# Kernel tuning notes

Measured on AMD Instinct MI355X. Metric: run time of the kernel, lower is better.

## Reference

```python
import jax, jax.numpy as jnp
import numpy as np

D = 1024

def setup_inputs() -> dict:
    key = jax.random.key(0)
    kx, kw = jax.random.split(key)
    x = jax.random.normal(kx, (4, 2048, D), dtype=jnp.float32)
    # nn.Linear(d, 3d, bias=False): weight [3d, d]; y = x @ W.T
    W = jax.random.normal(kw, (3 * D, D), dtype=jnp.float32) * (1.0 / np.sqrt(D))
    return {"x": x, "W": W}

def reference(x, W):
    d = x.shape[-1]
    qkv = jnp.einsum('bsd,ed->bse', x, W)  # [B,S,3d]
    q, k, v = jnp.split(qkv, 3, axis=2)
    att = jnp.einsum('bqd,bkd->bqk', q, k) * (1.0 / jnp.sqrt(jnp.asarray(d, x.dtype)))
    att = jax.nn.softmax(att, axis=-1)
    y = jnp.einsum('bqk,bkd->bqd', att, v)
    return y
```

## Files before the change

kernel.cpp:

```cpp
#include <hip/hip_runtime.h>
#include <hip/hip_bf16.h>

typedef __attribute__((ext_vector_type(8))) short short8;
typedef __attribute__((ext_vector_type(4))) float f32x4;

typedef unsigned short u16;

__device__ __forceinline__ u16 f32_to_bf16(float f) {
    unsigned int u = __float_as_uint(f);
    u += 0x7fffu + ((u >> 16) & 1u);
    return (u16)(u >> 16);
}

__device__ __forceinline__ void gload16(const u16* g, u16* lds_base) {
    __builtin_amdgcn_global_load_lds(
        (const __attribute__((address_space(1))) void*)g,
        (__attribute__((address_space(3))) void*)lds_base, 16, 0, 0);
}

__device__ __forceinline__ void phase_bar() {
    __builtin_amdgcn_s_barrier();
    __builtin_amdgcn_sched_barrier(0);
}
__device__ __forceinline__ void wait_vm8() {
    asm volatile("s_waitcnt vmcnt(8)" ::: "memory");
    __builtin_amdgcn_sched_barrier(0);
}
__device__ __forceinline__ void wait_vm7() {
    asm volatile("s_waitcnt vmcnt(7)" ::: "memory");
    __builtin_amdgcn_sched_barrier(0);
}
__device__ __forceinline__ void wait_vm0() {
    asm volatile("s_waitcnt vmcnt(0)" ::: "memory");
    __builtin_amdgcn_sched_barrier(0);
}

__global__ void cast_inputs(const float* __restrict__ x, u16* __restrict__ Xb,
                            const float* __restrict__ W, u16* __restrict__ Wb,
                            float* __restrict__ l,
                            int nx4, int nw4, int nl) {
    int i = blockIdx.x * blockDim.x + threadIdx.x;
    if (i >= nx4 + nw4) {
        int idx = i - (nx4 + nw4);
        if (idx < nl) l[idx] = 0.f;
        return;
    }
    const float* in; u16* out; int idx;
    if (i < nx4) { in = x; out = Xb; idx = i; }
    else { idx = i - nx4; in = W; out = Wb; }
    float4 v = ((const float4*)in)[idx];
    ushort4 o;
    o.x = f32_to_bf16(v.x); o.y = f32_to_bf16(v.y);
    o.z = f32_to_bf16(v.z); o.w = f32_to_bf16(v.w);
    ((ushort4*)out)[idx] = o;
}


struct Acc256 { f32x4 acc[8][4]; };
struct Acc192 { f32x4 acc[8][3]; };

template<int MH>
__device__ __forceinline__ void rd_a(const u16* __restrict__ sA, int wr, int lane,
                                     int lr, short8 (&af)[4][2]) {
#pragma unroll
    for (int a2 = 0; a2 < 4; ++a2) {
        const int row = wr * 128 + MH * 64 + a2 * 16 + lr;
#pragma unroll
        for (int k2 = 0; k2 < 2; ++k2) {
            const int cb = (lane >> 4) + k2 * 4;
            af[a2][k2] = *(const short8*)(sA + row * 64 + ((cb ^ (lr & 7)) * 8));
        }
    }
}

template<int NH>
__device__ __forceinline__ void rd_b(const u16* __restrict__ sB, int wc, int lane,
                                     int lr, short8 (&bf)[2][2]) {
#pragma unroll
    for (int b2 = 0; b2 < 2; ++b2) {
        const int row = wc * 64 + NH * 32 + b2 * 16 + lr;
#pragma unroll
        for (int k2 = 0; k2 < 2; ++k2) {
            const int cb = (lane >> 4) + k2 * 4;
            bf[b2][k2] = *(const short8*)(sB + row * 64 + ((cb ^ (lr & 7)) * 8));
        }
    }
}

template<int MH, int NH>
__device__ __forceinline__ void mm_q(Acc256& fr, const short8 (&af)[4][2],
                                     const short8 (&bf)[2][2]) {
    __builtin_amdgcn_s_setprio(1);
#pragma unroll
    for (int a2 = 0; a2 < 4; ++a2)
#pragma unroll
        for (int b2 = 0; b2 < 2; ++b2)
#pragma unroll
            for (int k2 = 0; k2 < 2; ++k2)
                fr.acc[MH * 4 + a2][NH * 2 + b2] =
                    __builtin_amdgcn_mfma_f32_16x16x32_bf16(
                        af[a2][k2], bf[b2][k2],
                        fr.acc[MH * 4 + a2][NH * 2 + b2], 0, 0, 0);
    __builtin_amdgcn_s_setprio(0);
}

__device__ __forceinline__ void rd_b01(const u16* __restrict__ sB, int wc, int lane,
                                       int lr, short8 (&bf)[2][2]) {
#pragma unroll
    for (int b2 = 0; b2 < 2; ++b2) {
        const int row = wc * 48 + b2 * 16 + lr;
#pragma unroll
        for (int k2 = 0; k2 < 2; ++k2) {
            const int cb = (lane >> 4) + k2 * 4;
            bf[b2][k2] = *(const short8*)(sB + row * 64 + ((cb ^ (lr & 7)) * 8));
        }
    }
}

__device__ __forceinline__ void rd_b2(const u16* __restrict__ sB, int wc, int lane,
                                      int lr, short8 (&bf)[2]) {
    const int row = wc * 48 + 32 + lr;
#pragma unroll
    for (int k2 = 0; k2 < 2; ++k2) {
        const int cb = (lane >> 4) + k2 * 4;
        bf[k2] = *(const short8*)(sB + row * 64 + ((cb ^ (lr & 7)) * 8));
    }
}

template<int MH>
__device__ __forceinline__ void mm_b01(Acc192& fr, const short8 (&af)[4][2],
                                       const short8 (&bf)[2][2]) {
    __builtin_amdgcn_s_setprio(1);
#pragma unroll
    for (int a2 = 0; a2 < 4; ++a2)
#pragma unroll
        for (int b2 = 0; b2 < 2; ++b2)
#pragma unroll
            for (int k2 = 0; k2 < 2; ++k2)
                fr.acc[MH * 4 + a2][b2] =
                    __builtin_amdgcn_mfma_f32_16x16x32_bf16(
                        af[a2][k2], bf[b2][k2],
                        fr.acc[MH * 4 + a2][b2], 0, 0, 0);
    __builtin_amdgcn_s_setprio(0);
}

template<int MH>
__device__ __forceinline__ void mm_b2(Acc192& fr, const short8 (&af)[4][2],
                                      const short8 (&bf)[2]) {
    __builtin_amdgcn_s_setprio(1);
#pragma unroll
    for (int a2 = 0; a2 < 4; ++a2)
#pragma unroll
        for (int k2 = 0; k2 < 2; ++k2)
            fr.acc[MH * 4 + a2][2] =
                __builtin_amdgcn_mfma_f32_16x16x32_bf16(
                    af[a2][k2], bf[k2], fr.acc[MH * 4 + a2][2], 0, 0, 0);
    __builtin_amdgcn_s_setprio(0);
}

__device__ __forceinline__ void gemm_core_256(
    const u16* __restrict__ A, const u16* __restrict__ Bt,
    int K, int lda, int ldb, int row0, int col0, u16* sm, Acc256& fr)
{
    const int t    = threadIdx.x;
    const int lane = t & 63;
    const int wave = t >> 6;
    const int wr   = wave >> 2;
    const int wc   = wave & 3;
    const int lr   = lane & 15;
    const int srow = lane >> 3;
    const int gc   = (lane & 7) ^ srow;

    const u16* const sA0 = sm;
    const u16* const sA1 = sm + 16384;
    const u16* const sB0 = sm + 32768;
    const u16* const sB1 = sm + 49152;

#pragma unroll
    for (int a = 0; a < 8; ++a)
#pragma unroll
        for (int b = 0; b < 4; ++b)
            fr.acc[a][b] = (f32x4){0.f, 0.f, 0.f, 0.f};

    const u16* aB = A  + (long long)(row0 + wave * 8 + srow) * lda + gc * 8;
    const u16* bB = Bt + (long long)(col0 + wave * 8 + srow) * ldb + gc * 8;
    u16* const sAw = sm + wave * 512;
    u16* const sBw = sm + 32768 + wave * 512;

    auto stageA = [&](int kt) {
        u16* d = sAw + (kt & 1) * 16384;
        const u16* g = aB + kt * 64;
#pragma unroll
        for (int r4 = 0; r4 < 4; ++r4)
            gload16(g + (long long)(r4 * 64) * lda, d + r4 * 4096);
    };
    auto stageB = [&](int kt) {
        u16* d = sBw + (kt & 1) * 16384;
        const u16* g = bB + kt * 64;
#pragma unroll
        for (int r4 = 0; r4 < 4; ++r4)
            gload16(g + (long long)(r4 * 64) * ldb, d + r4 * 4096);
    };

    stageA(0); stageB(0); stageA(1); stageB(1);
    wait_vm8();
    phase_bar();

    const int NI = K >> 7;
    short8 af[4][2], bfa[2][2], bfb[2][2];
#pragma unroll 1
    for (int i = 0; i < NI; ++i) {
        const bool more = (i + 1 < NI);
        const int t2 = 2 * i + 2;

        rd_a<0>(sA0, wr, lane, lr, af);
        rd_b<0>(sB0, wc, lane, lr, bfa);
        phase_bar();
        mm_q<0, 0>(fr, af, bfa);
        phase_bar();

        rd_b<1>(sB0, wc, lane, lr, bfb);
        phase_bar();
        mm_q<0, 1>(fr, af, bfb);
        phase_bar();

        rd_a<1>(sA0, wr, lane, lr, af);
        if (more) stageB(t2);
        phase_bar();
        mm_q<1, 1>(fr, af, bfb);
        phase_bar();

        if (more) stageA(t2);
        phase_bar();
        mm_q<1, 0>(fr, af, bfa);
        if (more) wait_vm8(); else wait_vm0();
        phase_bar();

        rd_a<0>(sA1, wr, lane, lr, af);
        rd_b<0>(sB1, wc, lane, lr, bfa);
        phase_bar();
        mm_q<0, 0>(fr, af, bfa);
        phase_bar();

        rd_b<1>(sB1, wc, lane, lr, bfb);
        phase_bar();
        mm_q<0, 1>(fr, af, bfb);
        phase_bar();

        rd_a<1>(sA1, wr, lane, lr, af);
        if (more) stageB(t2 + 1);
        phase_bar();
        mm_q<1, 1>(fr, af, bfb);
        phase_bar();

        if (more) stageA(t2 + 1);
        phase_bar();
        mm_q<1, 0>(fr, af, bfa);
        if (more) wait_vm8();
        phase_bar();
    }
}

__device__ __forceinline__ void gemm_core_192(
    const u16* __restrict__ A, const u16* __restrict__ Bt,
    int K, int lda, int ldb, int row0, int col0, u16* sm, Acc192& fr)
{
    const int t    = threadIdx.x;
    const int lane = t & 63;
    const int wave = t >> 6;
    const int wr   = wave >> 2;
    const int wc   = wave & 3;
    const int lr   = lane & 15;
    const int srow = lane >> 3;
    const int gc   = (lane & 7) ^ srow;

    const u16* const sA0 = sm;
    const u16* const sA1 = sm + 16384;
    const u16* const sB0 = sm + 32768;
    const u16* const sB1 = sm + 45056;

#pragma unroll
    for (int a = 0; a < 8; ++a)
#pragma unroll
        for (int b = 0; b < 3; ++b)
            fr.acc[a][b] = (f32x4){0.f, 0.f, 0.f, 0.f};

    const u16* aB = A  + (long long)(row0 + wave * 8 + srow) * lda + gc * 8;
    const u16* bB = Bt + (long long)(col0 + wave * 8 + srow) * ldb + gc * 8;
    u16* const sAw = sm + wave * 512;
    u16* const sBw = sm + 32768 + wave * 512;

    auto stageA = [&](int kt) {
        u16* d = sAw + (kt & 1) * 16384;
        const u16* g = aB + kt * 64;
#pragma unroll
        for (int r4 = 0; r4 < 4; ++r4)
            gload16(g + (long long)(r4 * 64) * lda, d + r4 * 4096);
    };
    auto stageB = [&](int kt) {
        u16* d = sBw + (kt & 1) * 12288;
        const u16* g = bB + kt * 64;
#pragma unroll
        for (int r4 = 0; r4 < 3; ++r4)
            gload16(g + (long long)(r4 * 64) * ldb, d + r4 * 4096);
    };

    stageA(0); stageB(0); stageA(1); stageB(1);
    wait_vm7();
    phase_bar();

    const int NI = K >> 7;
    short8 af[4][2], bfa[2][2], bfb[2];
#pragma unroll 1
    for (int i = 0; i < NI; ++i) {
        const bool more = (i + 1 < NI);
        const int t2 = 2 * i + 2;

        rd_a<0>(sA0, wr, lane, lr, af);
        rd_b01(sB0, wc, lane, lr, bfa);
        phase_bar();
        mm_b01<0>(fr, af, bfa);
        phase_bar();

        rd_b2(sB0, wc, lane, lr, bfb);
        phase_bar();
        mm_b2<0>(fr, af, bfb);
        phase_bar();

        rd_a<1>(sA0, wr, lane, lr, af);
        if (more) stageB(t2);
        phase_bar();
        mm_b2<1>(fr, af, bfb);
        phase_bar();

        if (more) stageA(t2);
        phase_bar();
        mm_b01<1>(fr, af, bfa);
        if (more) wait_vm7(); else wait_vm0();
        phase_bar();

        rd_a<0>(sA1, wr, lane, lr, af);
        rd_b01(sB1, wc, lane, lr, bfa);
        phase_bar();
        mm_b01<0>(fr, af, bfa);
        phase_bar();

        rd_b2(sB1, wc, lane, lr, bfb);
        phase_bar();
        mm_b2<0>(fr, af, bfb);
        phase_bar();

        rd_a<1>(sA1, wr, lane, lr, af);
        if (more) stageB(t2 + 1);
        phase_bar();
        mm_b2<1>(fr, af, bfb);
        phase_bar();

        if (more) stageA(t2 + 1);
        phase_bar();
        mm_b01<1>(fr, af, bfa);
        if (more) wait_vm7();
        phase_bar();
    }
}


__global__ __launch_bounds__(512, 1) void gemm_qkv(
    const u16* __restrict__ Xb, const u16* __restrict__ Wb,
    u16* __restrict__ QK, u16* __restrict__ VT)
{
    __shared__ u16 sm[57344];
    const int row0 = blockIdx.y * 256;
    const int col0 = blockIdx.x * 192;

    Acc192 fr;
    gemm_core_192(Xb, Wb, 1024, 1024, 1024, row0, col0, sm, fr);

    const int lane = threadIdx.x & 63;
    const int wave = threadIdx.x >> 6;
    const int wr = wave >> 2, wc = wave & 3;
    const int cr = (lane >> 4) * 4, cc = lane & 15;

#pragma unroll
    for (int a = 0; a < 8; ++a) {
        const int grow = row0 + wr * 128 + a * 16 + cr;
#pragma unroll
        for (int b = 0; b < 3; ++b) {
            const int gcol = col0 + wc * 48 + b * 16 + cc;
            if (gcol < 2048) {
#pragma unroll
                for (int r = 0; r < 4; ++r)
                    QK[(long long)(grow + r) * 2048 + gcol] =
                        f32_to_bf16(fr.acc[a][b][r]);
            } else {
                const int bz = grow >> 11, s = grow & 2047;
                const int d = gcol - 2048;
                ushort4 o;
                o.x = f32_to_bf16(fr.acc[a][b][0]);
                o.y = f32_to_bf16(fr.acc[a][b][1]);
                o.z = f32_to_bf16(fr.acc[a][b][2]);
                o.w = f32_to_bf16(fr.acc[a][b][3]);
                *(ushort4*)(&VT[((long long)(bz * 1024 + d)) * 2048 + s]) = o;
            }
        }
    }
}

__global__ __launch_bounds__(512, 1) void gemm_s_exp(
    const u16* __restrict__ QK, u16* __restrict__ E, float* __restrict__ l)
{
    __shared__ u16 sm[65536];
    const long long boff = (long long)blockIdx.z * 2048 * 2048;
    const u16* Q  = QK + boff;
    const u16* Kp = QK + boff + 1024;
    u16* Eb = E + boff;
    float* lb = l + (long long)blockIdx.z * 2048;
    const int row0 = blockIdx.y * 256;
    const int col0 = blockIdx.x * 256;

    Acc256 fr;
    gemm_core_256(Q, Kp, 1024, 2048, 2048, row0, col0, sm, fr);

    const int lane = threadIdx.x & 63;
    const int wave = threadIdx.x >> 6;
    const int wr = wave >> 2, wc = wave & 3;
    const int cr = (lane >> 4) * 4, cc = lane & 15;

#pragma unroll
    for (int a = 0; a < 8; ++a) {
        float rs[4] = {0.f, 0.f, 0.f, 0.f};
#pragma unroll
        for (int b = 0; b < 4; ++b)
#pragma unroll
            for (int r = 0; r < 4; ++r) {
                float e = __expf(fr.acc[a][b][r] * 0.03125f);
                rs[r] += e;
                int grow = row0 + wr * 128 + a * 16 + cr + r;
                int gcol = col0 + wc * 64 + b * 16 + cc;
                Eb[(long long)grow * 2048 + gcol] = f32_to_bf16(e);
            }
#pragma unroll
        for (int r = 0; r < 4; ++r) {
#pragma unroll
            for (int m = 1; m < 16; m <<= 1) rs[r] += __shfl_xor(rs[r], m, 64);
            if ((lane & 15) == 0)
                atomicAdd(&lb[row0 + wr * 128 + a * 16 + cr + r], rs[r]);
        }
    }
}


struct Frag128 { f32x4 acc[4][4]; int lane, wm, wn; };

__device__ __forceinline__ void gemm_core_128(
    const u16* __restrict__ A, const u16* __restrict__ Bt, int K, int lda, int ldb,
    int row0, int col0, u16* sA, u16* sB, Frag128& fr)
{
    const int t    = threadIdx.x;
    const int lane = t & 63;
    const int wave = t >> 6;
    fr.lane = lane;
    fr.wm = (wave >> 1) * 64;
    fr.wn = (wave & 1) * 64;
    const int lr = lane & 15;

#pragma unroll
    for (int i = 0; i < 4; ++i)
#pragma unroll
        for (int j = 0; j < 4; ++j)
            fr.acc[i][j] = (f32x4){0.f, 0.f, 0.f, 0.f};

    const int srow = lane >> 3;
    const int gc   = (lane & 7) ^ srow;
    for (int k0 = 0; k0 < K; k0 += 64) {
        __syncthreads();
#pragma unroll
        for (int c = 0; c < 4; ++c) {
            const int rb = c * 32 + wave * 8;
            const int r  = rb + srow;
            gload16(A  + (long long)(row0 + r) * lda + k0 + gc * 8, &sA[rb * 64]);
            gload16(Bt + (long long)(col0 + r) * ldb + k0 + gc * 8, &sB[rb * 64]);
        }
        __syncthreads();

#pragma unroll
        for (int kk = 0; kk < 64; kk += 32) {
            const int cb = (lane >> 4) + (kk >> 3);
            const int sl = (cb ^ (lr & 7)) * 8;
            short8 af[4], bf[4];
#pragma unroll
            for (int i = 0; i < 4; ++i) {
                af[i] = *(const short8*)(&sA[(fr.wm + i * 16 + lr) * 64 + sl]);
                bf[i] = *(const short8*)(&sB[(fr.wn + i * 16 + lr) * 64 + sl]);
            }
#pragma unroll
            for (int i = 0; i < 4; ++i)
#pragma unroll
                for (int j = 0; j < 4; ++j)
                    fr.acc[i][j] = __builtin_amdgcn_mfma_f32_16x16x32_bf16(
                        af[i], bf[j], fr.acc[i][j], 0, 0, 0);
        }
    }
}

__global__ __launch_bounds__(256) void gemm_pv_ts(
    const u16* __restrict__ E, const u16* __restrict__ VT,
    const float* __restrict__ l, float* __restrict__ Y)
{
    __shared__ u16 sA[128 * 64];
    __shared__ u16 sB[128 * 64];
    const u16* VTb = VT + (long long)blockIdx.z * 1024 * 2048;
    const u16* Eb  = E  + (long long)blockIdx.z * 2048 * 2048;
    const float* lb = l + (long long)blockIdx.z * 2048;
    float* Yb = Y + (long long)blockIdx.z * 2048 * 1024;
    const int row0 = blockIdx.y * 128;
    const int col0 = blockIdx.x * 128;
    Frag128 fr;
    gemm_core_128(VTb, Eb, 2048, 2048, 2048, row0, col0, sA, sB, fr);
    const int cr = (fr.lane >> 4) * 4, cc = fr.lane & 15;
#pragma unroll
    for (int j = 0; j < 4; ++j) {
        int q = col0 + fr.wn + j * 16 + cc;
        float inv = 1.0f / lb[q];
#pragma unroll
        for (int i = 0; i < 4; ++i) {
            int d = row0 + fr.wm + i * 16 + cr;
            float4 o = {fr.acc[i][j][0] * inv, fr.acc[i][j][1] * inv,
                        fr.acc[i][j][2] * inv, fr.acc[i][j][3] * inv};
            *(float4*)(&Yb[(long long)q * 1024 + d]) = o;
        }
    }
}

extern "C" void kernel_launch(void* const* d_in, const int* in_sizes, int n_in,
                              void* d_out, int out_size, void* d_ws, size_t ws_size,
                              hipStream_t stream) {
    const float* x = (const float*)d_in[0];
    const float* W = (const float*)d_in[1];
    float* out = (float*)d_out;

    char* ws = (char*)d_ws;
    u16*   Xb = (u16*)(ws);
    u16*   Wb = (u16*)(ws + 16777216LL);
    u16*   QK = (u16*)(ws + 23068672LL);
    u16*   VT = (u16*)(ws + 56623104LL);
    u16*   E  = (u16*)(ws + 73400320LL);
    float* l  = (float*)(ws + 106954752LL);

    const int nx4 = 8192 * 1024 / 4, nw4 = 3072 * 1024 / 4;
    cast_inputs<<<11296, 256, 0, stream>>>(x, Xb, W, Wb, l, nx4, nw4, 8192);
    gemm_qkv<<<dim3(16, 32, 1), 512, 0, stream>>>(Xb, Wb, QK, VT);
    gemm_s_exp<<<dim3(8, 8, 4), 512, 0, stream>>>(QK, E, l);
    gemm_pv_ts<<<dim3(16, 8, 4), 256, 0, stream>>>(E, VT, l, out);
}
```

Measured before the change: 240.0 us.

## Use 256x256 split-K PV GEMM with partial buffers and separate reduce

```diff
diff --git a/kernel.cpp b/kernel.cpp
--- a/kernel.cpp
+++ b/kernel.cpp
@@ -449,87 +449,50 @@
     }
 }
 
-
-struct Frag128 { f32x4 acc[4][4]; int lane, wm, wn; };
-
-__device__ __forceinline__ void gemm_core_128(
-    const u16* __restrict__ A, const u16* __restrict__ Bt, int K, int lda, int ldb,
-    int row0, int col0, u16* sA, u16* sB, Frag128& fr)
+__global__ __launch_bounds__(512, 1) void gemm_pv_sk(
+    const u16* __restrict__ E, const u16* __restrict__ VT,
+    float* __restrict__ P0, float* __restrict__ P1)
 {
-    const int t    = threadIdx.x;
-    const int lane = t & 63;
-    const int wave = t >> 6;
-    fr.lane = lane;
-    fr.wm = (wave >> 1) * 64;
-    fr.wn = (wave & 1) * 64;
-    const int lr = lane & 15;
-
-#pragma unroll
-    for (int i = 0; i < 4; ++i)
-#pragma unroll
-        for (int j = 0; j < 4; ++j)
-            fr.acc[i][j] = (f32x4){0.f, 0.f, 0.f, 0.f};
-
-    const int srow = lane >> 3;
-    const int gc   = (lane & 7) ^ srow;
-    for (int k0 = 0; k0 < K; k0 += 64) {
-        __syncthreads();
-#pragma unroll
-        for (int c = 0; c < 4; ++c) {
-            const int rb = c * 32 + wave * 8;
-            const int r  = rb + srow;
-            gload16(A  + (long long)(row0 + r) * lda + k0 + gc * 8, &sA[rb * 64]);
-            gload16(Bt + (long long)(col0 + r) * ldb + k0 + gc * 8, &sB[rb * 64]);
+    __shared__ u16 sm[65536];
+    const int qt = blockIdx.x;
+    const int dt = blockIdx.y & 3;
+    const int ks = blockIdx.y >> 2;
+    const u16* Eb  = E  + (long long)blockIdx.z * 2048 * 2048 + ks * 1024;
+    const u16* VTb = VT + (long long)blockIdx.z * 1024 * 2048 + ks * 1024;
+    float* Pb = (ks ? P1 : P0) + (long long)blockIdx.z * 2048 * 1024;
+
+    Acc256 fr;
+    gemm_core_256(Eb, VTb, 1024, 2048, 2048, qt * 256, dt * 256, sm, fr);
+
+    const int lane = threadIdx.x & 63;
+    const int wave = threadIdx.x >> 6;
+    const int wr = wave >> 2, wc = wave & 3;
+    const int cr = (lane >> 4) * 4, cc = lane & 15;
+#pragma unroll
+    for (int a = 0; a < 8; ++a) {
+        const int q = qt * 256 + wr * 128 + a * 16 + cr;
+#pragma unroll
+        for (int b = 0; b < 4; ++b) {
+            const int d = dt * 256 + wc * 64 + b * 16 + cc;
+#pragma unroll
+            for (int r = 0; r < 4; ++r)
+                Pb[(long long)(q + r) * 1024 + d] = fr.acc[a][b][r];
         }
-        __syncthreads();
-
-#pragma unroll
-        for (int kk = 0; kk < 64; kk += 32) {
-            const int cb = (lane >> 4) + (kk >> 3);
-            const int sl = (cb ^ (lr & 7)) * 8;
-            short8 af[4], bf[4];
-#pragma unroll
-            for (int i = 0; i < 4; ++i) {
-                af[i] = *(const short8*)(&sA[(fr.wm + i * 16 + lr) * 64 + sl]);
-                bf[i] = *(const short8*)(&sB[(fr.wn + i * 16 + lr) * 64 + sl]);
-            }
-#pragma unroll
-            for (int i = 0; i < 4; ++i)
-#pragma unroll
-                for (int j = 0; j < 4; ++j)
-                    fr.acc[i][j] = __builtin_amdgcn_mfma_f32_16x16x32_bf16(
-                        af[i], bf[j], fr.acc[i][j], 0, 0, 0);
-        }
-    }
-}
-
-__global__ __launch_bounds__(256) void gemm_pv_ts(
-    const u16* __restrict__ E, const u16* __restrict__ VT,
-    const float* __restrict__ l, float* __restrict__ Y)
-{
-    __shared__ u16 sA[128 * 64];
-    __shared__ u16 sB[128 * 64];
-    const u16* VTb = VT + (long long)blockIdx.z * 1024 * 2048;
-    const u16* Eb  = E  + (long long)blockIdx.z * 2048 * 2048;
-    const float* lb = l + (long long)blockIdx.z * 2048;
-    float* Yb = Y + (long long)blockIdx.z * 2048 * 1024;
-    const int row0 = blockIdx.y * 128;
-    const int col0 = blockIdx.x * 128;
-    Frag128 fr;
-    gemm_core_128(VTb, Eb, 2048, 2048, 2048, row0, col0, sA, sB, fr);
-    const int cr = (fr.lane >> 4) * 4, cc = fr.lane & 15;
-#pragma unroll
-    for (int j = 0; j < 4; ++j) {
-        int q = col0 + fr.wn + j * 16 + cc;
-        float inv = 1.0f / lb[q];
-#pragma unroll
-        for (int i = 0; i < 4; ++i) {
-            int d = row0 + fr.wm + i * 16 + cr;
-            float4 o = {fr.acc[i][j][0] * inv, fr.acc[i][j][1] * inv,
-                        fr.acc[i][j][2] * inv, fr.acc[i][j][3] * inv};
-            *(float4*)(&Yb[(long long)q * 1024 + d]) = o;
-        }
-    }
+    }
+}
+
+__global__ void reduce_pv(float* __restrict__ out, const float* __restrict__ part,
+                          const float* __restrict__ l) {
+    const int i = blockIdx.x * blockDim.x + threadIdx.x;
+    const int e0 = i << 2;
+    const int q  = (e0 >> 10) & 2047;
+    const int z  = e0 >> 21;
+    const float linv = 1.0f / l[z * 2048 + q];
+    float4 a = ((const float4*)out)[i];
+    float4 b = ((const float4*)part)[i];
+    float4 o = {(a.x + b.x) * linv, (a.y + b.y) * linv,
+                (a.z + b.z) * linv, (a.w + b.w) * linv};
+    ((float4*)out)[i] = o;
 }
 
 extern "C" void kernel_launch(void* const* d_in, const int* in_sizes, int n_in,
@@ -551,5 +514,6 @@
     cast_inputs<<<11296, 256, 0, stream>>>(x, Xb, W, Wb, l, nx4, nw4, 8192);
     gemm_qkv<<<dim3(16, 32, 1), 512, 0, stream>>>(Xb, Wb, QK, VT);
     gemm_s_exp<<<dim3(8, 8, 4), 512, 0, stream>>>(QK, E, l);
-    gemm_pv_ts<<<dim3(16, 8, 4), 256, 0, stream>>>(E, VT, l, out);
-}
+    gemm_pv_sk<<<dim3(8, 8, 4), 512, 0, stream>>>(E, VT, out, (float*)QK);
+    reduce_pv<<<8192, 256, 0, stream>>>(out, (float*)QK, l);
+}
```

Result: no change. 244.1 us (+1.7%).
